# Optimization experiments

Hardware: AMD Instinct MI355X
Metric: run time of the kernel (lower is better)

The kernel has to match this reference:

```python
import jax, jax.numpy as jnp
import numpy as np

N, E, F_IN = 50000, 300000, 128
BN_EPS = 1e-5


def setup_inputs() -> dict:
    key = jax.random.key(0)
    ks = jax.random.split(key, 8)
    inp = {
        "x": jax.random.normal(ks[0], (N, F_IN), jnp.float32),
        "src": jax.random.randint(ks[1], (E,), 0, N),
        "dst": jax.random.randint(ks[2], (E,), 0, N),
    }
    dims = [(F_IN, 500), (500, 1000), (1000, 500), (500, 50)]
    for li, (a, b) in enumerate(dims, 1):
        kw = jax.random.fold_in(ks[3], li)
        scale = 1.0 / np.sqrt(a)
        inp[f"W{li}"] = jax.random.uniform(kw, (a, b), jnp.float32, -scale, scale)
        inp[f"b{li}"] = jnp.zeros((b,), jnp.float32)
        if li < 4:
            inp[f"g{li}"] = jnp.ones((b,), jnp.float32)
            inp[f"be{li}"] = jnp.zeros((b,), jnp.float32)
    return inp


def _gcn(x, W, b, src, dst, edge_norm, self_norm):
    # GCNConv: h = X W; out = sum_{(s->d)} norm * h[s] + self_loop + bias
    h = x @ W  # [N, out]
    agg = jax.ops.segment_sum(h[src] * edge_norm[:, None], dst, num_segments=N)
    return agg + h * self_norm[:, None] + b


def _bn(x, g, be):
    # BatchNorm1d training-mode statistics over the node dim (biased var, as torch)
    m = jnp.mean(x, axis=0)
    v = jnp.mean(jnp.square(x - m), axis=0)
    return g * (x - m) * jax.lax.rsqrt(v + BN_EPS) + be


def reference(x, src, dst, W1, b1, g1, be1, W2, b2, g2, be2, W3, b3, g3, be3, W4, b4):
    # symmetric normalization with self-loops: deg over targets (incl. self-loop)
    deg = jax.ops.segment_sum(jnp.ones((E,), jnp.float32), dst, num_segments=N) + 1.0
    dis = jax.lax.rsqrt(deg)
    edge_norm = dis[src] * dis[dst]
    self_norm = dis * dis
    h = jax.nn.elu(_gcn(x, W1, b1, src, dst, edge_norm, self_norm))
    h = _bn(h, g1, be1)
    h = jax.nn.elu(_gcn(h, W2, b2, src, dst, edge_norm, self_norm))
    h = _bn(h, g2, be2)
    h = jax.nn.elu(_gcn(h, W3, b3, src, dst, edge_norm, self_norm))
    h = _bn(h, g3, be3)
    return _gcn(h, W4, b4, src, dst, edge_norm, self_norm)
```

## Files before the change

### kernel.cpp

```cpp
#include <hip/hip_runtime.h>
#include <hip/hip_bf16.h>
#include <cstdint>
#include <cstddef>

#define NN 50000
#define NE 300000
#define BN_EPS 1e-5f

typedef unsigned short ushort_t;
typedef __attribute__((ext_vector_type(8))) short short8;
typedef __attribute__((ext_vector_type(4))) float f32x4;

__device__ __forceinline__ float bf_to_f(ushort_t u) {
    union { unsigned int i; float f; } c; c.i = ((unsigned int)u) << 16; return c.f;
}
__device__ __forceinline__ ushort_t f_to_bf(float f) {
    union { unsigned int i; float f; } c; c.f = f;
    unsigned int r = c.i + 0x7FFF + ((c.i >> 16) & 1);
    return (ushort_t)(r >> 16);
}
__device__ __forceinline__ void from_f(float& d, float v) { d = v; }
__device__ __forceinline__ void from_f(ushort_t& d, float v) { d = f_to_bf(v); }

__global__ void deg_kernel(const int* __restrict__ dst, int* __restrict__ deg, int E) {
    int e = blockIdx.x * blockDim.x + threadIdx.x;
    if (e < E) atomicAdd(&deg[dst[e]], 1);
}

__global__ void scan_reduce(const int* __restrict__ deg, int* __restrict__ bsum,
                            float* __restrict__ dis, int n) {
    int tid = threadIdx.x;
    int idx = blockIdx.x * 256 + tid;
    int v = (idx < n) ? deg[idx] : 0;
    if (idx < n) dis[idx] = rsqrtf((float)v + 1.0f);
    __shared__ int sh[256];
    sh[tid] = v;
    __syncthreads();
    #pragma unroll
    for (int off = 128; off > 0; off >>= 1) {
        if (tid < off) sh[tid] += sh[tid + off];
        __syncthreads();
    }
    if (tid == 0) bsum[blockIdx.x] = sh[0];
}

__global__ void scan_offsets(const int* __restrict__ bsum, int* __restrict__ boff,
                             int* __restrict__ rowstart, int nb, int n) {
    __shared__ int sh[256];
    int tid = threadIdx.x;
    int v = (tid < nb) ? bsum[tid] : 0;
    sh[tid] = v;
    __syncthreads();
    #pragma unroll
    for (int off = 1; off < 256; off <<= 1) {
        int t = (tid >= off) ? sh[tid - off] : 0;
        __syncthreads();
        sh[tid] += t;
        __syncthreads();
    }
    if (tid < nb) boff[tid] = sh[tid] - v;
    if (tid == nb - 1) rowstart[n] = sh[tid];
}

__global__ void scan_final(const int* __restrict__ deg, const int* __restrict__ boff,
                           int* __restrict__ rowstart, int n) {
    int tid = threadIdx.x;
    int idx = blockIdx.x * 256 + tid;
    int v = (idx < n) ? deg[idx] : 0;
    __shared__ int sh[256];
    sh[tid] = v;
    __syncthreads();
    #pragma unroll
    for (int off = 1; off < 256; off <<= 1) {
        int t = (tid >= off) ? sh[tid - off] : 0;
        __syncthreads();
        sh[tid] += t;
        __syncthreads();
    }
    if (idx < n) rowstart[idx] = boff[blockIdx.x] + sh[tid] - v;
}

__global__ void fill_kernel(const int* __restrict__ src, const int* __restrict__ dst,
                            const int* __restrict__ rowstart, int* __restrict__ cnt,
                            int* __restrict__ esrc, float* __restrict__ ew,
                            const float* __restrict__ dis, int E) {
    int e = blockIdx.x * blockDim.x + threadIdx.x;
    if (e >= E) return;
    int s = src[e], d = dst[e];
    int pos = rowstart[d] + atomicAdd(&cnt[d], 1);
    esrc[pos] = s;
    ew[pos] = dis[s] * dis[d];
}

__global__ void wt_kernel(const float* __restrict__ W, ushort_t* __restrict__ WT,
                          int K, int N, int KP, int NP) {
    int i = blockIdx.x * 256 + threadIdx.x;
    int total = NP * KP;
    if (i >= total) return;
    int n = i / KP, k = i - n * KP;
    float v = (k < K && n < N) ? W[(size_t)k * N + n] : 0.f;
    WT[i] = f_to_bf(v);
}

__global__ __launch_bounds__(256) void gather_x(
        const float* __restrict__ in, ushort_t* __restrict__ out,
        const int* __restrict__ rowstart, const int* __restrict__ esrc,
        const float* __restrict__ ew, const float* __restrict__ dis, int nnodes) {
    int gw = (blockIdx.x * 256 + threadIdx.x) >> 6;
    if (gw >= nnodes) return;
    int lane = threadIdx.x & 63;
    int c0 = lane * 2;
    int j0 = rowstart[gw], j1 = rowstart[gw + 1];
    float dn = dis[gw], sw = dn * dn;
    float2 v0 = *(const float2*)(in + (size_t)gw * 128 + c0);
    float a0 = v0.x * sw, a1 = v0.y * sw;
    for (int j = j0; j < j1; ++j) {
        int s = esrc[j];
        float w = ew[j];
        float2 u = *(const float2*)(in + (size_t)s * 128 + c0);
        a0 = fmaf(w, u.x, a0);
        a1 = fmaf(w, u.y, a1);
    }
    unsigned int packed = (unsigned int)f_to_bf(a0) | ((unsigned int)f_to_bf(a1) << 16);
    *(unsigned int*)(out + (size_t)gw * 128 + c0) = packed;
}

__global__ __launch_bounds__(256) void gather_b8(
        const ushort_t* __restrict__ in, ushort_t* __restrict__ out,
        const int* __restrict__ rowstart, const int* __restrict__ esrc,
        const float* __restrict__ ew, const float* __restrict__ dis,
        const float* __restrict__ scale, const float* __restrict__ shift,
        const float* __restrict__ bias, int F, int do_elu, int nnodes) {
    int gw = (blockIdx.x * 256 + threadIdx.x) >> 6;
    if (gw >= nnodes) return;
    int lane = threadIdx.x & 63;
    int c0 = lane * 8;
    int j0 = rowstart[gw], j1 = rowstart[gw + 1];
    float dn = dis[gw], sw = dn * dn;
    float sc[8], sh[8], bs[8];
    #pragma unroll
    for (int k = 0; k < 8; ++k) {
        sc[k] = scale ? scale[c0 + k] : 1.f;
        sh[k] = scale ? shift[c0 + k] : 0.f;
        bs[k] = (bias && c0 + k < F) ? bias[c0 + k] : 0.f;
    }
    float acc[8];
    {
        short8 u = *(const short8*)(in + (size_t)gw * 512 + c0);
        #pragma unroll
        for (int k = 0; k < 8; ++k)
            acc[k] = fmaf(bf_to_f((ushort_t)u[k]), sc[k], sh[k]) * sw;
    }
    for (int j = j0; j < j1; ++j) {
        int s = esrc[j];
        float w = ew[j];
        short8 u = *(const short8*)(in + (size_t)s * 512 + c0);
        #pragma unroll
        for (int k = 0; k < 8; ++k)
            acc[k] = fmaf(w, fmaf(bf_to_f((ushort_t)u[k]), sc[k], sh[k]), acc[k]);
    }
    short8 o;
    #pragma unroll
    for (int k = 0; k < 8; ++k) {
        float v = 0.f;
        if (c0 + k < F) {
            v = acc[k] + bs[k];
            if (do_elu) v = v > 0.f ? v : expm1f(v);
        }
        o[k] = (short)f_to_bf(v);
    }
    *(short8*)(out + (size_t)gw * 512 + c0) = o;
}

__global__ __launch_bounds__(256) void gather_out(
        const float* __restrict__ in, float* __restrict__ out,
        const int* __restrict__ rowstart, const int* __restrict__ esrc,
        const float* __restrict__ ew, const float* __restrict__ dis,
        const float* __restrict__ bias, int nnodes) {
    int gw = (blockIdx.x * 256 + threadIdx.x) >> 6;
    if (gw >= nnodes) return;
    int lane = threadIdx.x & 63;
    int j0 = rowstart[gw], j1 = rowstart[gw + 1];
    float dn = dis[gw], sw = dn * dn;
    float a = 0.f;
    if (lane < 50) a = in[(size_t)gw * 64 + lane] * sw;
    for (int j = j0; j < j1; ++j) {
        int s = esrc[j];
        float w = ew[j];
        if (lane < 50) a = fmaf(w, in[(size_t)s * 64 + lane], a);
    }
    if (lane < 50) out[(size_t)gw * 50 + lane] = a + bias[lane];
}

template <typename TC>
__global__ __launch_bounds__(256) void mfma_gemm(
        const ushort_t* __restrict__ A, const ushort_t* __restrict__ WT,
        const float* __restrict__ bias,
        const float* __restrict__ scale, const float* __restrict__ shift,
        TC* __restrict__ C,
        int M, int KP, int N, int CP, int do_elu) {
    __shared__ ushort_t As[128][40];
    __shared__ ushort_t Bs[64][40];
    int bm = blockIdx.x * 128;
    int bn = blockIdx.y * 64;
    int tid = threadIdx.x;
    int lane = tid & 63, wid = tid >> 6;
    int wr = wid >> 1, wc = wid & 1;
    int rl = lane & 15, kg = lane >> 4;
    f32x4 acc[4][2] = {};

    for (int k0 = 0; k0 < KP; k0 += 32) {
        #pragma unroll
        for (int it = 0; it < 2; ++it) {
            int s = tid + it * 256;
            int r = s >> 2, q = s & 3;
            int grow = bm + r;
            union { int4 v; ushort_t h[8]; } u;
            if (grow < M) u.v = *(const int4*)(A + (size_t)grow * KP + k0 + q * 8);
            else u.v = make_int4(0, 0, 0, 0);
            if (scale) {
                #pragma unroll
                for (int j = 0; j < 8; ++j) {
                    int k = k0 + q * 8 + j;
                    u.h[j] = f_to_bf(fmaf(bf_to_f(u.h[j]), scale[k], shift[k]));
                }
            }
            *(int4*)&As[r][q * 8] = u.v;
        }
        {
            int r = tid >> 2, q = tid & 3;
            *(int4*)&Bs[r][q * 8] = *(const int4*)(WT + (size_t)(bn + r) * KP + k0 + q * 8);
        }
        __syncthreads();
        short8 av[4], bv[2];
        #pragma unroll
        for (int mi = 0; mi < 4; ++mi)
            av[mi] = *(const short8*)&As[wr * 64 + mi * 16 + rl][kg * 8];
        #pragma unroll
        for (int ni = 0; ni < 2; ++ni)
            bv[ni] = *(const short8*)&Bs[wc * 32 + ni * 16 + rl][kg * 8];
        #pragma unroll
        for (int mi = 0; mi < 4; ++mi)
            #pragma unroll
            for (int ni = 0; ni < 2; ++ni)
                acc[mi][ni] = __builtin_amdgcn_mfma_f32_16x16x32_bf16(
                    av[mi], bv[ni], acc[mi][ni], 0, 0, 0);
        __syncthreads();
    }
    #pragma unroll
    for (int mi = 0; mi < 4; ++mi) {
        #pragma unroll
        for (int ni = 0; ni < 2; ++ni) {
            int col = bn + wc * 32 + ni * 16 + rl;
            #pragma unroll
            for (int r = 0; r < 4; ++r) {
                int row = bm + wr * 64 + mi * 16 + kg * 4 + r;
                if (row >= M) continue;
                float v = 0.f;
                if (col < N) {
                    v = acc[mi][ni][r];
                    if (bias) v += bias[col];
                    if (do_elu) v = v > 0.f ? v : expm1f(v);
                }
                from_f(C[(size_t)row * CP + col], v);
            }
        }
    }
}

#define CS_ROWS 128
__global__ void colstats_kernel(const ushort_t* __restrict__ h, float* __restrict__ sum,
                                float* __restrict__ sumsq, int M, int F, int FP) {
    int r0 = blockIdx.x * CS_ROWS;
    int tid = threadIdx.x;
    float s[4] = {0.f, 0.f, 0.f, 0.f}, q[4] = {0.f, 0.f, 0.f, 0.f};
    int rend = min(r0 + CS_ROWS, M);
    for (int r = r0; r < rend; ++r) {
        #pragma unroll
        for (int j = 0; j < 4; ++j) {
            int c = tid + j * 256;
            if (c < F) {
                float v = bf_to_f(h[(size_t)r * FP + c]);
                s[j] += v;
                q[j] += v * v;
            }
        }
    }
    #pragma unroll
    for (int j = 0; j < 4; ++j) {
        int c = tid + j * 256;
        if (c < F) {
            atomicAdd(&sum[c], s[j]);
            atomicAdd(&sumsq[c], q[j]);
        }
    }
}

__global__ void bnparams_kernel(const float* __restrict__ sum, const float* __restrict__ sumsq,
                                const float* __restrict__ g, const float* __restrict__ be,
                                float* __restrict__ scale, float* __restrict__ shift,
                                int F, int FP, float invN) {
    int c = blockIdx.x * blockDim.x + threadIdx.x;
    if (c >= FP) return;
    if (c >= F) { scale[c] = 0.f; shift[c] = 0.f; return; }
    float m = sum[c] * invN;
    float v = sumsq[c] * invN - m * m;
    if (v < 0.f) v = 0.f;
    float sc = g[c] * rsqrtf(v + BN_EPS);
    scale[c] = sc;
    shift[c] = be[c] - m * sc;
}

extern "C" void kernel_launch(void* const* d_in, const int* in_sizes, int n_in,
                              void* d_out, int out_size, void* d_ws, size_t ws_size,
                              hipStream_t stream) {
    const float* x  = (const float*)d_in[0];
    const int* src  = (const int*)d_in[1];
    const int* dst  = (const int*)d_in[2];
    const float* W1 = (const float*)d_in[3];
    const float* b1 = (const float*)d_in[4];
    const float* g1 = (const float*)d_in[5];
    const float* be1= (const float*)d_in[6];
    const float* W2 = (const float*)d_in[7];
    const float* b2 = (const float*)d_in[8];
    const float* g2 = (const float*)d_in[9];
    const float* be2= (const float*)d_in[10];
    const float* W3 = (const float*)d_in[11];
    const float* b3 = (const float*)d_in[12];
    const float* g3 = (const float*)d_in[13];
    const float* be3= (const float*)d_in[14];
    const float* W4 = (const float*)d_in[15];
    const float* b4 = (const float*)d_in[16];
    float* out = (float*)d_out;

    char* ws = (char*)d_ws;
    int*   deg      = (int*)ws;
    int*   cnt      = deg + NN;
    int*   rowstart = cnt + NN;
    float* dis      = (float*)(rowstart + NN + 1);
    float* sum      = (float*)(ws + (800 << 10));
    float* sumsq    = sum + 4096;
    float* scale    = sum + 8192;
    float* shift    = sum + 12288;
    int*   bsum     = (int*)(shift + 4096);
    int*   boff     = bsum + 256;
    int*   esrc     = (int*)(ws + (1 << 20));
    float* ew       = (float*)(ws + 2359296);
    ushort_t* wt1 = (ushort_t*)(ws + (4u << 20));
    ushort_t* wt2 = (ushort_t*)(ws + (4u << 20) + (512u << 10));
    ushort_t* wt3 = (ushort_t*)(ws + (4u << 20) + (1664u << 10));
    ushort_t* wt4 = (ushort_t*)(ws + (4u << 20) + (2816u << 10));
    char* base = ws + (8u << 20);
    const size_t R50 = 52428800;
    ushort_t* regA  = (ushort_t*)base;
    ushort_t* regBC = (ushort_t*)(base + R50);

    if (ws_size < (8u << 20) + 3 * R50) return;

    const float invN = 1.0f / (float)NN;
    const int NB = (NN + 255) / 256;
    const int GW = (NN * 64 + 255) / 256;
    const int GM = (NN + 127) / 128;

    (void)hipMemsetAsync(deg, 0, 2 * NN * sizeof(int), stream);
    deg_kernel<<<(NE + 255) / 256, 256, 0, stream>>>(dst, deg, NE);
    scan_reduce<<<NB, 256, 0, stream>>>(deg, bsum, dis, NN);
    scan_offsets<<<1, 256, 0, stream>>>(bsum, boff, rowstart, NB, NN);
    scan_final<<<NB, 256, 0, stream>>>(deg, boff, rowstart, NN);
    fill_kernel<<<(NE + 255) / 256, 256, 0, stream>>>(src, dst, rowstart, cnt, esrc, ew, dis, NE);
    wt_kernel<<<(512 * 128 + 255) / 256, 256, 0, stream>>>(W1, wt1, 128, 500, 128, 512);
    wt_kernel<<<(1024 * 512 + 255) / 256, 256, 0, stream>>>(W2, wt2, 500, 1000, 512, 1024);
    wt_kernel<<<(512 * 1024 + 255) / 256, 256, 0, stream>>>(W3, wt3, 1000, 500, 1024, 512);
    wt_kernel<<<(64 * 512 + 255) / 256, 256, 0, stream>>>(W4, wt4, 500, 50, 512, 64);

    gather_x<<<GW, 256, 0, stream>>>(x, regA, rowstart, esrc, ew, dis, NN);
    mfma_gemm<ushort_t><<<dim3(GM, 8), 256, 0, stream>>>(
        regA, wt1, b1, nullptr, nullptr, regBC, NN, 128, 500, 512, 1);
    (void)hipMemsetAsync(sum, 0, 8192 * sizeof(float), stream);
    colstats_kernel<<<(NN + CS_ROWS - 1) / CS_ROWS, 256, 0, stream>>>(regBC, sum, sumsq, NN, 500, 512);
    bnparams_kernel<<<2, 256, 0, stream>>>(sum, sumsq, g1, be1, scale, shift, 500, 512, invN);

    gather_b8<<<GW, 256, 0, stream>>>(
        regBC, regA, rowstart, esrc, ew, dis, scale, shift, nullptr, 500, 0, NN);
    mfma_gemm<ushort_t><<<dim3(GM, 16), 256, 0, stream>>>(
        regA, wt2, b2, nullptr, nullptr, regBC, NN, 512, 1000, 1024, 1);
    (void)hipMemsetAsync(sum, 0, 8192 * sizeof(float), stream);
    colstats_kernel<<<(NN + CS_ROWS - 1) / CS_ROWS, 256, 0, stream>>>(regBC, sum, sumsq, NN, 1000, 1024);
    bnparams_kernel<<<4, 256, 0, stream>>>(sum, sumsq, g2, be2, scale, shift, 1000, 1024, invN);

    mfma_gemm<ushort_t><<<dim3(GM, 8), 256, 0, stream>>>(
        regBC, wt3, nullptr, scale, shift, regA, NN, 1024, 500, 512, 0);
    gather_b8<<<GW, 256, 0, stream>>>(
        regA, regBC, rowstart, esrc, ew, dis, nullptr, nullptr, b3, 500, 1, NN);
    (void)hipMemsetAsync(sum, 0, 8192 * sizeof(float), stream);
    colstats_kernel<<<(NN + CS_ROWS - 1) / CS_ROWS, 256, 0, stream>>>(regBC, sum, sumsq, NN, 500, 512);
    bnparams_kernel<<<2, 256, 0, stream>>>(sum, sumsq, g3, be3, scale, shift, 500, 512, invN);

    float* t4 = (float*)regA;
    mfma_gemm<float><<<dim3(GM, 1), 256, 0, stream>>>(
        regBC, wt4, nullptr, scale, shift, t4, NN, 512, 50, 64, 0);
    gather_out<<<GW, 256, 0, stream>>>(t4, out, rowstart, esrc, ew, dis, b4, NN);
}
```

Measured before the change: 1.200 ms.

## Fold BatchNorm into weights and use direct global-to-LDS loads in GEMM

BatchNorm scale is folded into the transposed bf16 weights, and the shift becomes a per-column vector c = shift·W. For layer 2 the aggregation is applied first, so the shift term is multiplied by a per-row dvec holding the sum of the normalized edge weights. This removes the per-element scale/shift work from the GEMM A-tile load and from the gather. The GEMM tile grows to 128x128 with a flat LDS buffer loaded through global_load_lds, and the grid axes are swapped so N tiles vary fastest. Risks: A rows are no longer bounds-checked, so the last M tile reads past row 50000 into the workspace, and the wt4 padding to 128 rows may overflow its slot.

```diff
diff --git a/kernel.cpp b/kernel.cpp
--- a/kernel.cpp
+++ b/kernel.cpp
@@ -6,6 +6,7 @@
 #define NN 50000
 #define NE 300000
 #define BN_EPS 1e-5f
+#define USE_GLL 1
 
 typedef unsigned short ushort_t;
 typedef __attribute__((ext_vector_type(8))) short short8;
@@ -92,14 +93,32 @@
     ew[pos] = dis[s] * dis[d];
 }
 
-__global__ void wt_kernel(const float* __restrict__ W, ushort_t* __restrict__ WT,
-                          int K, int N, int KP, int NP) {
+__global__ void dvec_kernel(const int* __restrict__ rowstart, const float* __restrict__ ew,
+                            const float* __restrict__ dis, float* __restrict__ d, int n) {
     int i = blockIdx.x * 256 + threadIdx.x;
-    int total = NP * KP;
-    if (i >= total) return;
+    if (i >= n) return;
+    float s = dis[i] * dis[i];
+    for (int j = rowstart[i]; j < rowstart[i + 1]; ++j) s += ew[j];
+    d[i] = s;
+}
+
+__global__ void wtscale_kernel(const float* __restrict__ W, const float* __restrict__ scale,
+                               ushort_t* __restrict__ WT, int K, int N, int KP, int NP) {
+    int i = blockIdx.x * 256 + threadIdx.x;
+    if (i >= NP * KP) return;
     int n = i / KP, k = i - n * KP;
     float v = (k < K && n < N) ? W[(size_t)k * N + n] : 0.f;
+    if (scale && k < K) v *= scale[k];
     WT[i] = f_to_bf(v);
+}
+
+__global__ void cvec_kernel(const float* __restrict__ W, const float* __restrict__ shift,
+                            float* __restrict__ c, int K, int N) {
+    int n = blockIdx.x * 256 + threadIdx.x;
+    if (n >= N) return;
+    float s = 0.f;
+    for (int k = 0; k < K; ++k) s += shift[k] * W[(size_t)k * N + n];
+    c[n] = s;
 }
 
 __global__ __launch_bounds__(256) void gather_x(
@@ -129,7 +148,6 @@
         const ushort_t* __restrict__ in, ushort_t* __restrict__ out,
         const int* __restrict__ rowstart, const int* __restrict__ esrc,
         const float* __restrict__ ew, const float* __restrict__ dis,
-        const float* __restrict__ scale, const float* __restrict__ shift,
         const float* __restrict__ bias, int F, int do_elu, int nnodes) {
     int gw = (blockIdx.x * 256 + threadIdx.x) >> 6;
     if (gw >= nnodes) return;
@@ -137,34 +155,25 @@
     int c0 = lane * 8;
     int j0 = rowstart[gw], j1 = rowstart[gw + 1];
     float dn = dis[gw], sw = dn * dn;
-    float sc[8], sh[8], bs[8];
-    #pragma unroll
-    for (int k = 0; k < 8; ++k) {
-        sc[k] = scale ? scale[c0 + k] : 1.f;
-        sh[k] = scale ? shift[c0 + k] : 0.f;
-        bs[k] = (bias && c0 + k < F) ? bias[c0 + k] : 0.f;
-    }
     float acc[8];
     {
         short8 u = *(const short8*)(in + (size_t)gw * 512 + c0);
         #pragma unroll
-        for (int k = 0; k < 8; ++k)
-            acc[k] = fmaf(bf_to_f((ushort_t)u[k]), sc[k], sh[k]) * sw;
+        for (int k = 0; k < 8; ++k) acc[k] = bf_to_f((ushort_t)u[k]) * sw;
     }
     for (int j = j0; j < j1; ++j) {
         int s = esrc[j];
         float w = ew[j];
         short8 u = *(const short8*)(in + (size_t)s * 512 + c0);
         #pragma unroll
-        for (int k = 0; k < 8; ++k)
-            acc[k] = fmaf(w, fmaf(bf_to_f((ushort_t)u[k]), sc[k], sh[k]), acc[k]);
+        for (int k = 0; k < 8; ++k) acc[k] = fmaf(w, bf_to_f((ushort_t)u[k]), acc[k]);
     }
     short8 o;
     #pragma unroll
     for (int k = 0; k < 8; ++k) {
         float v = 0.f;
         if (c0 + k < F) {
-            v = acc[k] + bs[k];
+            v = acc[k] + (bias ? bias[c0 + k] : 0.f);
             if (do_elu) v = v > 0.f ? v : expm1f(v);
         }
         o[k] = (short)f_to_bf(v);
@@ -195,71 +204,77 @@
 template <typename TC>
 __global__ __launch_bounds__(256) void mfma_gemm(
         const ushort_t* __restrict__ A, const ushort_t* __restrict__ WT,
-        const float* __restrict__ bias,
-        const float* __restrict__ scale, const float* __restrict__ shift,
+        const float* __restrict__ bias, const float* __restrict__ cvec,
+        const float* __restrict__ dvec,
         TC* __restrict__ C,
         int M, int KP, int N, int CP, int do_elu) {
-    __shared__ ushort_t As[128][40];
-    __shared__ ushort_t Bs[64][40];
-    int bm = blockIdx.x * 128;
-    int bn = blockIdx.y * 64;
+    __shared__ ushort_t lds[8192];
+    int bn = blockIdx.x * 128;
+    int bm = blockIdx.y * 128;
     int tid = threadIdx.x;
     int lane = tid & 63, wid = tid >> 6;
     int wr = wid >> 1, wc = wid & 1;
     int rl = lane & 15, kg = lane >> 4;
-    f32x4 acc[4][2] = {};
+    f32x4 acc[4][4] = {};
 
     for (int k0 = 0; k0 < KP; k0 += 32) {
         #pragma unroll
-        for (int it = 0; it < 2; ++it) {
-            int s = tid + it * 256;
-            int r = s >> 2, q = s & 3;
-            int grow = bm + r;
-            union { int4 v; ushort_t h[8]; } u;
-            if (grow < M) u.v = *(const int4*)(A + (size_t)grow * KP + k0 + q * 8);
-            else u.v = make_int4(0, 0, 0, 0);
-            if (scale) {
-                #pragma unroll
-                for (int j = 0; j < 8; ++j) {
-                    int k = k0 + q * 8 + j;
-                    u.h[j] = f_to_bf(fmaf(bf_to_f(u.h[j]), scale[k], shift[k]));
-                }
-            }
-            *(int4*)&As[r][q * 8] = u.v;
-        }
-        {
-            int r = tid >> 2, q = tid & 3;
-            *(int4*)&Bs[r][q * 8] = *(const int4*)(WT + (size_t)(bn + r) * KP + k0 + q * 8);
-        }
-        __syncthreads();
-        short8 av[4], bv[2];
+        for (int i = 0; i < 2; ++i) {
+            int sb = (wid * 2 + i) * 64;
+            int slot = sb + lane;
+            int r = slot >> 2, q = slot & 3;
+            const ushort_t* ga = A + (size_t)(bm + r) * KP + k0 + q * 8;
+            const ushort_t* gb = WT + (size_t)(bn + r) * KP + k0 + q * 8;
+#if USE_GLL
+            __builtin_amdgcn_global_load_lds(
+                (const __attribute__((address_space(1))) unsigned int*)ga,
+                (__attribute__((address_space(3))) unsigned int*)&lds[sb * 8], 16, 0, 0);
+            __builtin_amdgcn_global_load_lds(
+                (const __attribute__((address_space(1))) unsigned int*)gb,
+                (__attribute__((address_space(3))) unsigned int*)&lds[4096 + sb * 8], 16, 0, 0);
+#else
+            *(int4*)&lds[slot * 8] = *(const int4*)ga;
+            *(int4*)&lds[4096 + slot * 8] = *(const int4*)gb;
+#endif
+        }
+#if USE_GLL
+        asm volatile("s_waitcnt vmcnt(0)" ::: "memory");
+#endif
+        __syncthreads();
+        short8 av[4], bv[4];
         #pragma unroll
         for (int mi = 0; mi < 4; ++mi)
-            av[mi] = *(const short8*)&As[wr * 64 + mi * 16 + rl][kg * 8];
-        #pragma unroll
-        for (int ni = 0; ni < 2; ++ni)
-            bv[ni] = *(const short8*)&Bs[wc * 32 + ni * 16 + rl][kg * 8];
+            av[mi] = *(const short8*)&lds[(wr * 64 + mi * 16 + rl) * 32 + kg * 8];
+        #pragma unroll
+        for (int ni = 0; ni < 4; ++ni)
+            bv[ni] = *(const short8*)&lds[4096 + (wc * 64 + ni * 16 + rl) * 32 + kg * 8];
         #pragma unroll
         for (int mi = 0; mi < 4; ++mi)
             #pragma unroll
-            for (int ni = 0; ni < 2; ++ni)
+            for (int ni = 0; ni < 4; ++ni)
                 acc[mi][ni] = __builtin_amdgcn_mfma_f32_16x16x32_bf16(
                     av[mi], bv[ni], acc[mi][ni], 0, 0, 0);
         __syncthreads();
     }
     #pragma unroll
-    for (int mi = 0; mi < 4; ++mi) {
-        #pragma unroll
-        for (int ni = 0; ni < 2; ++ni) {
-            int col = bn + wc * 32 + ni * 16 + rl;
+    for (int ni = 0; ni < 4; ++ni) {
+        int col = bn + wc * 64 + ni * 16 + rl;
+        if (col >= CP) continue;
+        float bb = 0.f, cc = 0.f;
+        if (col < N) {
+            bb = bias ? bias[col] : 0.f;
+            cc = cvec ? cvec[col] : 0.f;
+        }
+        #pragma unroll
+        for (int mi = 0; mi < 4; ++mi) {
             #pragma unroll
             for (int r = 0; r < 4; ++r) {
                 int row = bm + wr * 64 + mi * 16 + kg * 4 + r;
                 if (row >= M) continue;
                 float v = 0.f;
                 if (col < N) {
-                    v = acc[mi][ni][r];
-                    if (bias) v += bias[col];
+                    float dr = dvec ? dvec[row] : 1.f;
+                    v = acc[mi][ni][r] + bb + dr * cc;
                     if (do_elu) v = v > 0.f ? v : expm1f(v);
                 }
                 from_f(C[(size_t)row * CP + col], v);
@@ -344,8 +359,10 @@
     float* shift    = sum + 12288;
     int*   bsum     = (int*)(shift + 4096);
     int*   boff     = bsum + 256;
+    float* cv       = (float*)(ws + (880 << 10));
     int*   esrc     = (int*)(ws + (1 << 20));
     float* ew       = (float*)(ws + 2359296);
+    float* dvec     = (float*)(ws + (3520u << 10));
     ushort_t* wt1 = (ushort_t*)(ws + (4u << 20));
     ushort_t* wt2 = (ushort_t*)(ws + (4u << 20) + (512u << 10));
     ushort_t* wt3 = (ushort_t*)(ws + (4u << 20) + (1664u << 10));
@@ -368,36 +385,40 @@
     scan_offsets<<<1, 256, 0, stream>>>(bsum, boff, rowstart, NB, NN);
     scan_final<<<NB, 256, 0, stream>>>(deg, boff, rowstart, NN);
     fill_kernel<<<(NE + 255) / 256, 256, 0, stream>>>(src, dst, rowstart, cnt, esrc, ew, dis, NE);
-    wt_kernel<<<(512 * 128 + 255) / 256, 256, 0, stream>>>(W1, wt1, 128, 500, 128, 512);
-    wt_kernel<<<(1024 * 512 + 255) / 256, 256, 0, stream>>>(W2, wt2, 500, 1000, 512, 1024);
-    wt_kernel<<<(512 * 1024 + 255) / 256, 256, 0, stream>>>(W3, wt3, 1000, 500, 1024, 512);
-    wt_kernel<<<(64 * 512 + 255) / 256, 256, 0, stream>>>(W4, wt4, 500, 50, 512, 64);
+    dvec_kernel<<<NB, 256, 0, stream>>>(rowstart, ew, dis, dvec, NN);
+    wtscale_kernel<<<(512 * 128 + 255) / 256, 256, 0, stream>>>(W1, nullptr, wt1, 128, 500, 128, 512);
 
     gather_x<<<GW, 256, 0, stream>>>(x, regA, rowstart, esrc, ew, dis, NN);
-    mfma_gemm<ushort_t><<<dim3(GM, 8), 256, 0, stream>>>(
+    mfma_gemm<ushort_t><<<dim3(4, GM), 256, 0, stream>>>(
         regA, wt1, b1, nullptr, nullptr, regBC, NN, 128, 500, 512, 1);
     (void)hipMemsetAsync(sum, 0, 8192 * sizeof(float), stream);
     colstats_kernel<<<(NN + CS_ROWS - 1) / CS_ROWS, 256, 0, stream>>>(regBC, sum, sumsq, NN, 500, 512);
     bnparams_kernel<<<2, 256, 0, stream>>>(sum, sumsq, g1, be1, scale, shift, 500, 512, invN);
 
+    wtscale_kernel<<<(1024 * 512 + 255) / 256, 256, 0, stream>>>(W2, scale, wt2, 500, 1000, 512, 1024);
+    cvec_kernel<<<4, 256, 0, stream>>>(W2, shift, cv, 500, 1000);
     gather_b8<<<GW, 256, 0, stream>>>(
-        regBC, regA, rowstart, esrc, ew, dis, scale, shift, nullptr, 500, 0, NN);
-    mfma_gemm<ushort_t><<<dim3(GM, 16), 256, 0, stream>>>(
-        regA, wt2, b2, nullptr, nullptr, regBC, NN, 512, 1000, 1024, 1);
+        regBC, regA, rowstart, esrc, ew, dis, nullptr, 500, 0, NN);
+    mfma_gemm<ushort_t><<<dim3(8, GM), 256, 0, stream>>>(
+        regA, wt2, b2, cv, dvec, regBC, NN, 512, 1000, 1024, 1);
     (void)hipMemsetAsync(sum, 0, 8192 * sizeof(float), stream);
     colstats_kernel<<<(NN + CS_ROWS - 1) / CS_ROWS, 256, 0, stream>>>(regBC, sum, sumsq, NN, 1000, 1024);
     bnparams_kernel<<<4, 256, 0, stream>>>(sum, sumsq, g2, be2, scale, shift, 1000, 1024, invN);
 
-    mfma_gemm<ushort_t><<<dim3(GM, 8), 256, 0, stream>>>(
-        regBC, wt3, nullptr, scale, shift, regA, NN, 1024, 500, 512, 0);
+    wtscale_kernel<<<(512 * 1024 + 255) / 256, 256, 0, stream>>>(W3, scale, wt3, 1000, 500, 1024, 512);
+    cvec_kernel<<<2, 256, 0, stream>>>(W3, shift, cv, 1000, 500);
+    mfma_gemm<ushort_t><<<dim3(4, GM), 256, 0, stream>>>(
+        regBC, wt3, nullptr, cv, nullptr, regA, NN, 1024, 500, 512, 0);
     gather_b8<<<GW, 256, 0, stream>>>(
-        regA, regBC, rowstart, esrc, ew, dis, nullptr, nullptr, b3, 500, 1, NN);
+        regA, regBC, rowstart, esrc, ew, dis, b3, 500, 1, NN);
     (void)hipMemsetAsync(sum, 0, 8192 * sizeof(float), stream);
     colstats_kernel<<<(NN + CS_ROWS - 1) / CS_ROWS, 256, 0, stream>>>(regBC, sum, sumsq, NN, 500, 512);
     bnparams_kernel<<<2, 256, 0, stream>>>(sum, sumsq, g3, be3, scale, shift, 500, 512, invN);
 
+    wtscale_kernel<<<(128 * 512 + 255) / 256, 256, 0, stream>>>(W4, scale, wt4, 500, 50, 512, 128);
+    cvec_kernel<<<1, 256, 0, stream>>>(W4, shift, cv, 500, 50);
     float* t4 = (float*)regA;
-    mfma_gemm<float><<<dim3(GM, 1), 256, 0, stream>>>(
-        regBC, wt4, nullptr, scale, shift, t4, NN, 512, 50, 64, 0);
+    mfma_gemm<float><<<dim3(1, GM), 256, 0, stream>>>(
+        regBC, wt4, nullptr, cv, nullptr, t4, NN, 512, 50, 64, 0);
     gather_out<<<GW, 256, 0, stream>>>(t4, out, rowstart, esrc, ew, dis, b4, NN);
 }
```

After: 1.422 ms. 18.5% more time.
